# Kernel tuning notes

Measured on AMD Instinct MI355X. Metric: run time of the kernel, lower is better.

## Reference

```python
import jax, jax.numpy as jnp
import numpy as np
from jax.scipy.special import erf

# ---- physical constants (scipy.constants values; FIELD_CONSTANT in eV*Angstrom per e^2) ----
E_CHARGE = 1.602176634e-19
EPS0 = 8.8541878128e-12
PI = float(np.pi)
FIELD_CONSTANT = E_CHARGE * 1e10 / EPS0          # e/(eps0) with Angstrom length units
K_COUL = FIELD_CONSTANT / (4.0 * PI)             # ~14.3996 eV*A

# ---- module hyperparameters (from init_kwargs) ----
SIGMA_D = 0.5
SIGMAS = np.array([0.4, 0.8, 1.2, 1.6], dtype=np.float32)
NUM_RADIAL = 4
OFFSET = 0.1
N_PER_GRAPH = 128
NUM_GRAPHS = 32
M_NODES = N_PER_GRAPH * NUM_GRAPHS

# total_width_factors = sqrt((sigma_d^2 + sigma_r^2)/2)
W_FACTORS = np.sqrt((SIGMA_D**2 + SIGMAS**2) / 2.0).astype(np.float32)      # [R]
# multipole-normalized GTO: C_l = 1/(2^{l+1/2} sigma^{2l+3} Gamma(l+3/2)) => C1/C0 = 1/(3 sigma^2)
L0_FACTORS = np.ones(NUM_RADIAL, dtype=np.float32)                          # ratio = 1 under 'multipoles'
L1_FACTORS = (np.sqrt(3.0) * SIGMAS**2 * (1.0 / (3.0 * SIGMAS**2)) / OFFSET).astype(np.float32)

# 7 duplicate offsets: center, +x, +y, +z, -x, -y, -z
_h = OFFSET
OFFSETS7 = np.array([[0,0,0],[_h,0,0],[0,_h,0],[0,0,_h],[-_h,0,0],[0,-_h,0],[0,0,-_h]], dtype=np.float32)


def _duplicate_charges(sf):
    # sf: [M,4] -> [M,7] FD charge assignment (matches torch slot layout)
    t = 2.0 * OFFSET
    s0, s1, s2, s3 = sf[:, 0], sf[:, 1], sf[:, 2], sf[:, 3]
    return jnp.stack([s0, s3 / t, s1 / t, s2 / t, -s3 / t, -s1 / t, -s2 / t], axis=1)


def _project(sf7):
    # sf7: [M,7,R] per-duplicate scalar features -> [M, 4R]
    M = sf7.shape[0]
    l0 = jnp.asarray(L0_FACTORS) * sf7[:, 0]                                 # [M,R]
    half = 0.5 * jnp.asarray(L1_FACTORS)
    vy = half * (sf7[:, 2] - sf7[:, 5])   # column offset 0 in each triplet
    vz = half * (sf7[:, 3] - sf7[:, 6])   # column offset 1
    vx = half * (sf7[:, 1] - sf7[:, 4])   # column offset 2
    l1 = jnp.stack([vy, vz, vx], axis=-1).reshape(M, 3 * NUM_RADIAL)         # interleaved per radial
    return jnp.concatenate([l0, l1], axis=1)                                 # [M,4R]


def setup_inputs() -> dict:
    key = jax.random.key(0)
    k1, k2 = jax.random.split(key)
    source_feats = jax.random.normal(k1, (M_NODES, 1, 4), dtype=jnp.float32)
    node_positions = 4.0 * jax.random.normal(k2, (M_NODES, 3), dtype=jnp.float32)  # ~Angstrom scale
    batch = jnp.repeat(jnp.arange(NUM_GRAPHS, dtype=jnp.int64), N_PER_GRAPH)
    return {"source_feats": source_feats, "node_positions": node_positions, "batch": batch}


def reference(source_feats, node_positions, batch):
    # density_max_l=1, projection_max_l=1 -> call_density_1_feats_1 path.
    # Assumes equal-size graphs: batch = repeat(arange(G), n) (enforced by setup_inputs).
    sf = source_feats[:, 0, :]                                               # squeeze(-2): [M,4]
    M = sf.shape[0]
    G, n, D, R = NUM_GRAPHS, N_PER_GRAPH, 7 * N_PER_GRAPH, NUM_RADIAL
    w = jnp.asarray(W_FACTORS)                                               # [R]

    charges = _duplicate_charges(sf)                                         # [M,7]
    pos7 = node_positions[:, None, :] + jnp.asarray(OFFSETS7)[None]          # [M,7,3]

    pg = pos7.reshape(G, D, 3)
    cg = charges.reshape(G, D)

    diff = pg[:, :, None, :] - pg[:, None, :, :]                             # [G,D,D,3]
    d2 = jnp.sum(diff * diff, axis=-1)                                       # [G,D,D]
    orig = jnp.arange(D) // 7
    mask = (orig[:, None] != orig[None, :])                                  # exclude same-original-node pairs
    d = jnp.sqrt(jnp.where(mask, d2, 1.0))                                   # safe sqrt (masked entries dummy)
    smooth = erf(0.5 * d[..., None] / w) / (d[..., None] + 1e-6)             # [G,D,D,R]
    smooth = smooth * mask[None, :, :, None]
    # scatter_sum over senders i into receivers j
    sfeat = K_COUL * jnp.einsum('gi,gijr->gjr', cg, smooth)                  # [G,D,R]
    sfeat = sfeat.reshape(M, 7, R)

    # GTOSelfInteractionBlock (reconstructed): interactions among a node's own
    # 7 duplicates with analytic d->0 limit erf(x)/x -> 1/(w*sqrt(pi)).
    off = jnp.asarray(OFFSETS7)
    ds = jnp.linalg.norm(off[:, None, :] - off[None, :, :], axis=-1)          # [7,7]
    phi = jnp.where(ds[..., None] > 0.0,
                    erf(0.5 * ds[..., None] / w) / (ds[..., None] + 1e-6),
                    1.0 / (w * np.sqrt(PI)))                                  # [7,7,R]
    sself = K_COUL * jnp.einsum('mi,ijr->mjr', charges, phi)                  # [M,7,R]

    features = _project(sfeat)
    self_terms = _project(sself)
    features = features + self_terms                                          # include_self_interaction=True
    return features, self_terms
```

## Files before the change

### kernel.cpp

```cpp
#include <hip/hip_runtime.h>
#include <math.h>

namespace {

constexpr int   MTOT = 4096;
constexpr float H    = 0.1f;

constexpr float W0 = 0.45276925690687087f;
constexpr float W1 = 0.66708320320631664f;
constexpr float W2 = 0.91923881554251174f;
constexpr float W3 = 1.18532695911296985f;

constexpr float KCOUL   = 14.399645478425669f;
constexpr float HALF_L1 = 2.8867513459481287f;
constexpr float SQRTPI  = 1.7724538509055159f;

constexpr float K0 = 1.1043153f, K1 = 0.74953184f, K2 = 0.54392830f, K3 = 0.42182454f;

constexpr float PK0 = 0.5195472f, PK1 = 0.3526314f, PK2 = 0.2559019f, PK3 = 0.1984558f;
constexpr float C20 = -1.7593842f, C21 = -0.8105028f, C22 = -0.4268329f, C23 = -0.2567073f;
constexpr float EA1 = 0.3480242f, EA2 = -0.0958798f, EA3 = 0.7478556f;
constexpr float RCP_H = 9.9999000f, RCP_HS2 = 7.0710178f, RCP_2H = 4.9999750f;

constexpr int   TABN  = 512;
constexpr float TAB_H = 0.015f;
constexpr float INV_H = 66.666664f;

constexpr float SAT2 = 49.4f;

__device__ __forceinline__ float fast_rcp(float x)  { return __builtin_amdgcn_rcpf(x); }
__device__ __forceinline__ float fast_rsq(float x)  { return __builtin_amdgcn_rsqf(x); }
__device__ __forceinline__ float fast_exp2(float x) { return __builtin_amdgcn_exp2f(x); }

__device__ __forceinline__ float erf_q(float d, float d2, float pk, float c2) {
  float t = fast_rcp(__builtin_fmaf(d, pk, 1.0f));
  float poly = t * __builtin_fmaf(t, __builtin_fmaf(t, EA3, EA2), EA1);
  return poly * fast_exp2(d2 * c2);
}

__device__ __forceinline__ float project_one(const float* S, int k) {
  if (k < 4) return S[k];
  int q = k - 4;
  int r = q / 3;
  int comp = q - 3 * r;
  int j1, j2;
  if (comp == 0)      { j1 = 2; j2 = 5; }
  else if (comp == 1) { j1 = 3; j2 = 6; }
  else                { j1 = 1; j2 = 4; }
  return HALF_L1 * (S[j1 * 4 + r] - S[j2 * 4 + r]);
}

__device__ __forceinline__ unsigned spread3(int v) {
  return (unsigned)((v & 1) | ((v & 2) << 2) | ((v & 4) << 4));
}

__global__ __launch_bounds__(896, 4) void es_main(
    const float* __restrict__ sf,
    const float* __restrict__ pos,
    float* __restrict__ out)
{
  __shared__ float4   s_pos4[128];
  __shared__ float4   s_chg4[128];
  __shared__ int      s_orig[128];
  __shared__ unsigned s_key[128];
  __shared__ float4   s_tabV[TABN];
  __shared__ float4   s_tabD[TABN];
  __shared__ float    s_tmp[4][TABN + 1];
  __shared__ float4   s_part[8 * 112];
  __shared__ float    s_feat[448];
  __shared__ float    s_self[448];

  const int b   = blockIdx.x;
  const int g   = b >> 3;
  const int nb  = b & 7;
  const int tid = threadIdx.x;

  float px = 0.f, py = 0.f, pz = 0.f;
  float4 myc = make_float4(0.f, 0.f, 0.f, 0.f);
  if (tid < 128) {
    const float* p = pos + (size_t)(g * 128 + tid) * 3;
    px = p[0]; py = p[1]; pz = p[2];
    const float4 s = ((const float4*)sf)[g * 128 + tid];
    myc = make_float4(s.x, 5.0f * s.w, 5.0f * s.y, 5.0f * s.z);
    int cx = (int)((px + 16.0f) * 0.25f); cx = (cx < 0) ? 0 : (cx > 7 ? 7 : cx);
    int cy = (int)((py + 16.0f) * 0.25f); cy = (cy < 0) ? 0 : (cy > 7 ? 7 : cy);
    int cz = (int)((pz + 16.0f) * 0.25f); cz = (cz < 0) ? 0 : (cz > 7 ? 7 : cz);
    unsigned mort = spread3(cx) | (spread3(cy) << 1) | (spread3(cz) << 2);
    s_key[tid] = (mort << 7) | (unsigned)tid;
  }
  if (tid <= TABN) {
    const float d = tid * TAB_H;
    s_tmp[0][tid] = erff(K0 * d);
    s_tmp[1][tid] = erff(K1 * d);
    s_tmp[2][tid] = erff(K2 * d);
    s_tmp[3][tid] = erff(K3 * d);
  }
  __syncthreads();

  if (tid < 128) {
    const unsigned mykey = s_key[tid];
    int rank = 0;
    for (int t = 0; t < 128; ++t) rank += (s_key[t] < mykey) ? 1 : 0;
    s_pos4[rank] = make_float4(px, py, pz, 0.0f);
    s_chg4[rank] = myc;
    s_orig[rank] = tid;
  }
  if (tid < TABN) {
    const float v0 = s_tmp[0][tid], v1 = s_tmp[1][tid];
    const float v2v = s_tmp[2][tid], v3 = s_tmp[3][tid];
    s_tabV[tid] = make_float4(v0, v1, v2v, v3);
    s_tabD[tid] = make_float4(s_tmp[0][tid + 1] - v0, s_tmp[1][tid + 1] - v1,
                              s_tmp[2][tid + 1] - v2v, s_tmp[3][tid + 1] - v3);
  }
  __syncthreads();

  const int site_local = tid % 112;
  const int chunk      = tid / 112;
  const int sl   = nb * 112 + site_local;
  const int jown = (sl * 9363) >> 16;
  const int aoff = sl - jown * 7;

  const float4 cp = s_pos4[jown];
  const float tx = cp.x + ((aoff == 1) ? H : (aoff == 4) ? -H : 0.0f);
  const float ty = cp.y + ((aoff == 2) ? H : (aoff == 5) ? -H : 0.0f);
  const float tz = cp.z + ((aoff == 3) ? H : (aoff == 6) ? -H : 0.0f);

  float a0 = 0.f, a1 = 0.f, a2 = 0.f, a3 = 0.f, Ssat = 0.f;

  auto acc_full = [&](float d2raw, float c) {
    float d2 = fmaxf(d2raw, 1e-12f);
    float rd = fast_rsq(d2);
    float cv = c * rd;
    float t  = (d2 * rd) * INV_H;
    int  idx = (int)t;
    float f  = t - (float)idx;
    idx = (idx < TABN - 1) ? idx : (TABN - 1);
    f = fminf(f, 1.0f);
    const float4 V = s_tabV[idx];
    const float4 D = s_tabD[idx];
    a0 = __builtin_fmaf(cv, __builtin_fmaf(D.x, f, V.x), a0);
    a1 = __builtin_fmaf(cv, __builtin_fmaf(D.y, f, V.y), a1);
    a2 = __builtin_fmaf(cv, __builtin_fmaf(D.z, f, V.z), a2);
    a3 = __builtin_fmaf(cv, __builtin_fmaf(D.w, f, V.w), a3);
  };

  const int j0 = chunk * 16;
  for (int jj = 0; jj < 16; ++jj) {
    const int j = j0 + jj;
    const float4 p4 = s_pos4[j];
    const float4 c4 = s_chg4[j];
    const float vx = tx - p4.x;
    const float vy = ty - p4.y;
    const float vz = tz - p4.z;
    const float v2 = __builtin_fmaf(vx, vx, __builtin_fmaf(vy, vy, vz * vz));
    if (__any(v2 < SAT2)) {
      const float w2 = v2 + 0.01f;
      const bool own = (j == jown);
      acc_full(v2,                            (own & (aoff == 0)) ? 0.0f :  c4.x);
      acc_full(__builtin_fmaf(vx, -0.2f, w2), (own & (aoff == 1)) ? 0.0f :  c4.y);
      acc_full(__builtin_fmaf(vy, -0.2f, w2), (own & (aoff == 2)) ? 0.0f :  c4.z);
      acc_full(__builtin_fmaf(vz, -0.2f, w2), (own & (aoff == 3)) ? 0.0f :  c4.w);
      acc_full(__builtin_fmaf(vx,  0.2f, w2), (own & (aoff == 4)) ? 0.0f : -c4.y);
      acc_full(__builtin_fmaf(vy,  0.2f, w2), (own & (aoff == 5)) ? 0.0f : -c4.z);
      acc_full(__builtin_fmaf(vz,  0.2f, w2), (own & (aoff == 6)) ? 0.0f : -c4.w);
    } else {
      const float w2 = v2 + 0.01f;
      Ssat += c4.x * fast_rsq(v2);
      Ssat = __builtin_fmaf( c4.y, fast_rsq(__builtin_fmaf(vx, -0.2f, w2)), Ssat);
      Ssat = __builtin_fmaf( c4.z, fast_rsq(__builtin_fmaf(vy, -0.2f, w2)), Ssat);
      Ssat = __builtin_fmaf( c4.w, fast_rsq(__builtin_fmaf(vz, -0.2f, w2)), Ssat);
      Ssat = __builtin_fmaf(-c4.y, fast_rsq(__builtin_fmaf(vx,  0.2f, w2)), Ssat);
      Ssat = __builtin_fmaf(-c4.z, fast_rsq(__builtin_fmaf(vy,  0.2f, w2)), Ssat);
      Ssat = __builtin_fmaf(-c4.w, fast_rsq(__builtin_fmaf(vz,  0.2f, w2)), Ssat);
    }
  }
  a0 += Ssat; a1 += Ssat; a2 += Ssat; a3 += Ssat;

  s_part[chunk * 112 + site_local] = make_float4(a0, a1, a2, a3);
  __syncthreads();

  if (tid < 448) {
    const int site = tid >> 2;
    const int r    = tid & 3;
    const float* pf = (const float*)s_part;
    float tot = 0.f;
#pragma unroll
    for (int c = 0; c < 8; ++c) tot += pf[c * 448 + tid];

    const float w  = (r == 0) ? W0  : (r == 1) ? W1  : (r == 2) ? W2  : W3;
    const float pk = (r == 0) ? PK0 : (r == 1) ? PK1 : (r == 2) ? PK2 : PK3;
    const float c2 = (r == 0) ? C20 : (r == 1) ? C21 : (r == 2) ? C22 : C23;
    const float diag = fast_rcp(w * SQRTPI);
    const float ph1 = (1.f - erf_q(0.1f,        0.01f, pk, c2)) * RCP_H;
    const float ph2 = (1.f - erf_q(0.14142136f, 0.02f, pk, c2)) * RCP_HS2;
    const float ph3 = (1.f - erf_q(0.2f,        0.04f, pk, c2)) * RCP_2H;

    const int jn = (site * 9363) >> 16;
    const int ba = site - jn * 7;
    const float4 c4 = s_chg4[nb * 16 + jn];
    float selfSum = 0.f, ca = 0.f;
#pragma unroll
    for (int i = 0; i < 7; ++i) {
      const float ci = (i == 0) ?  c4.x : (i == 1) ?  c4.y : (i == 2) ?  c4.z :
                       (i == 3) ?  c4.w : (i == 4) ? -c4.y : (i == 5) ? -c4.z : -c4.w;
      float ph;
      if (i == ba)                             ph = diag;
      else if (i == 0 || ba == 0)              ph = ph1;
      else if ((i - ba == 3) || (ba - i == 3)) ph = ph3;
      else                                     ph = ph2;
      selfSum = __builtin_fmaf(ci, ph, selfSum);
      if (i == ba) ca = ci;
    }
    s_self[tid] = KCOUL * selfSum;
    s_feat[tid] = KCOUL * __builtin_fmaf(ca, diag, tot);
  }
  __syncthreads();

  if (tid < 256) {
    const int node = tid >> 4;
    const int k    = tid & 15;
    const int m    = g * 128 + s_orig[nb * 16 + node];
    float vf = project_one(&s_feat[node * 28], k);
    float vs = project_one(&s_self[node * 28], k);
    out[m * 16 + k]             = vf;
    out[MTOT * 16 + m * 16 + k] = vs;
  }
}

}

extern "C" void kernel_launch(void* const* d_in, const int* in_sizes, int n_in,
                              void* d_out, int out_size, void* d_ws, size_t ws_size,
                              hipStream_t stream) {
  const float* sf  = (const float*)d_in[0];
  const float* pos = (const float*)d_in[1];
  float* out = (float*)d_out;
  es_main<<<256, 896, 0, stream>>>(sf, pos, out);
}
```

Baseline: 75.21 us.

## Replace far-field duplicate sums with monopole-dipole expansion and tabulated kernels

```diff
diff --git a/kernel.cpp b/kernel.cpp
--- a/kernel.cpp
+++ b/kernel.cpp
@@ -14,6 +14,7 @@
 constexpr float KCOUL   = 14.399645478425669f;
 constexpr float HALF_L1 = 2.8867513459481287f;
 constexpr float SQRTPI  = 1.7724538509055159f;
+constexpr float TWOSQPI = 1.1283791670955126f;
 
 constexpr float K0 = 1.1043153f, K1 = 0.74953184f, K2 = 0.54392830f, K3 = 0.42182454f;
 
@@ -26,7 +27,12 @@
 constexpr float TAB_H = 0.015f;
 constexpr float INV_H = 66.666664f;
 
-constexpr float SAT2 = 49.4f;
+constexpr int   TGN   = 256;
+constexpr float TG_H  = 0.03f;
+constexpr float INV_G = 33.333332f;
+
+constexpr float NEAR2 = 4.0f;
+constexpr float SAT2  = 49.4f;
 
 __device__ __forceinline__ float fast_rcp(float x)  { return __builtin_amdgcn_rcpf(x); }
 __device__ __forceinline__ float fast_rsq(float x)  { return __builtin_amdgcn_rsqf(x); }
@@ -65,10 +71,14 @@
   __shared__ unsigned s_key[128];
   __shared__ float4   s_tabV[TABN];
   __shared__ float4   s_tabD[TABN];
-  __shared__ float    s_tmp[4][TABN + 1];
-  __shared__ float4   s_part[8 * 112];
+  __shared__ float4   s_gV[TGN], s_gD[TGN];
+  __shared__ float4   s_tV[TGN], s_tD[TGN];
+  __shared__ __align__(16) char s_u[8 * 112 * 16];
   __shared__ float    s_feat[448];
   __shared__ float    s_self[448];
+
+  float (*s_tmp)[TABN + 1] = reinterpret_cast<float (*)[TABN + 1]>(s_u);
+  float4* s_part = reinterpret_cast<float4*>(s_u);
 
   const int b   = blockIdx.x;
   const int g   = b >> 3;
@@ -94,6 +104,27 @@
     s_tmp[1][tid] = erff(K1 * d);
     s_tmp[2][tid] = erff(K2 * d);
     s_tmp[3][tid] = erff(K3 * d);
+  }
+  if (tid >= 640) {
+    const int e = tid - 640;
+    const float d0 = fmaxf(e * TG_H, 1e-3f);
+    const float d1 = (e + 1) * TG_H;
+    const float ks[4] = {K0, K1, K2, K3};
+    float gv[4], gd[4], tv[4], td[4];
+#pragma unroll
+    for (int r = 0; r < 4; ++r) {
+      const float k = ks[r];
+      const float e0 = erff(k * d0), e1 = erff(k * d1);
+      const float x0 = expf(-k * k * d0 * d0), x1 = expf(-k * k * d1 * d1);
+      const float g0 = e0 / d0, g1 = e1 / d1;
+      const float t0 = 0.2f * e0 / (d0 * d0 * d0) - 0.2f * TWOSQPI * k * x0 / (d0 * d0);
+      const float t1 = 0.2f * e1 / (d1 * d1 * d1) - 0.2f * TWOSQPI * k * x1 / (d1 * d1);
+      gv[r] = g0; gd[r] = g1 - g0; tv[r] = t0; td[r] = t1 - t0;
+    }
+    s_gV[e] = make_float4(gv[0], gv[1], gv[2], gv[3]);
+    s_gD[e] = make_float4(gd[0], gd[1], gd[2], gd[3]);
+    s_tV[e] = make_float4(tv[0], tv[1], tv[2], tv[3]);
+    s_tD[e] = make_float4(td[0], td[1], td[2], td[3]);
   }
   __syncthreads();
 
@@ -153,7 +184,7 @@
     const float vy = ty - p4.y;
     const float vz = tz - p4.z;
     const float v2 = __builtin_fmaf(vx, vx, __builtin_fmaf(vy, vy, vz * vz));
-    if (__any(v2 < SAT2)) {
+    if (__any(v2 < NEAR2)) {
       const float w2 = v2 + 0.01f;
       const bool own = (j == jown);
       acc_full(v2,                            (own & (aoff == 0)) ? 0.0f :  c4.x);
@@ -163,15 +194,37 @@
       acc_full(__builtin_fmaf(vx,  0.2f, w2), (own & (aoff == 4)) ? 0.0f : -c4.y);
       acc_full(__builtin_fmaf(vy,  0.2f, w2), (own & (aoff == 5)) ? 0.0f : -c4.z);
       acc_full(__builtin_fmaf(vz,  0.2f, w2), (own & (aoff == 6)) ? 0.0f : -c4.w);
+    } else if (__any(v2 < SAT2)) {
+      const float rd  = fast_rsq(v2);
+      const float d   = v2 * rd;
+      const float dot = __builtin_fmaf(c4.y, vx, __builtin_fmaf(c4.z, vy, c4.w * vz));
+      const float t   = d * INV_G;
+      const int   idx = (int)t;
+      const bool  in  = (idx < TGN - 1);
+      const int   ic  = in ? idx : (TGN - 2);
+      const float f   = fminf(t - (float)idx, 1.0f);
+      const float4 Gv = s_gV[ic], Gd = s_gD[ic];
+      const float4 Tv = s_tV[ic], Td = s_tD[ic];
+      const float rd2 = rd * rd;
+      const float gs  = rd;
+      const float ts  = 0.2f * rd2 * rd;
+      const float g0v = in ? __builtin_fmaf(Gd.x, f, Gv.x) : gs;
+      const float g1v = in ? __builtin_fmaf(Gd.y, f, Gv.y) : gs;
+      const float g2v = in ? __builtin_fmaf(Gd.z, f, Gv.z) : gs;
+      const float g3v = in ? __builtin_fmaf(Gd.w, f, Gv.w) : gs;
+      const float t0v = in ? __builtin_fmaf(Td.x, f, Tv.x) : ts;
+      const float t1v = in ? __builtin_fmaf(Td.y, f, Tv.y) : ts;
+      const float t2v = in ? __builtin_fmaf(Td.z, f, Tv.z) : ts;
+      const float t3v = in ? __builtin_fmaf(Td.w, f, Tv.w) : ts;
+      a0 = __builtin_fmaf(c4.x, g0v, __builtin_fmaf(dot, t0v, a0));
+      a1 = __builtin_fmaf(c4.x, g1v, __builtin_fmaf(dot, t1v, a1));
+      a2 = __builtin_fmaf(c4.x, g2v, __builtin_fmaf(dot, t2v, a2));
+      a3 = __builtin_fmaf(c4.x, g3v, __builtin_fmaf(dot, t3v, a3));
     } else {
-      const float w2 = v2 + 0.01f;
-      Ssat += c4.x * fast_rsq(v2);
-      Ssat = __builtin_fmaf( c4.y, fast_rsq(__builtin_fmaf(vx, -0.2f, w2)), Ssat);
-      Ssat = __builtin_fmaf( c4.z, fast_rsq(__builtin_fmaf(vy, -0.2f, w2)), Ssat);
-      Ssat = __builtin_fmaf( c4.w, fast_rsq(__builtin_fmaf(vz, -0.2f, w2)), Ssat);
-      Ssat = __builtin_fmaf(-c4.y, fast_rsq(__builtin_fmaf(vx,  0.2f, w2)), Ssat);
-      Ssat = __builtin_fmaf(-c4.z, fast_rsq(__builtin_fmaf(vy,  0.2f, w2)), Ssat);
-      Ssat = __builtin_fmaf(-c4.w, fast_rsq(__builtin_fmaf(vz,  0.2f, w2)), Ssat);
+      const float rd  = fast_rsq(v2);
+      const float dot = __builtin_fmaf(c4.y, vx, __builtin_fmaf(c4.z, vy, c4.w * vz));
+      Ssat = __builtin_fmaf(c4.x, rd, Ssat);
+      Ssat = __builtin_fmaf(0.2f * dot, rd * rd * rd, Ssat);
     }
   }
   a0 += Ssat; a1 += Ssat; a2 += Ssat; a3 += Ssat;
```

Result: faster. 70.34 us (-6.5%).
